# Kernel tuning notes

Measured on AMD Instinct MI355X. Metric: run time of the kernel, lower is better.

The kernel has to match this reference:

```python
import jax, jax.numpy as jnp
import numpy as np

B, S, H = 2, 1024, 4096
NH, NKV, HD = 32, 8, 128
GROUPS = NH // NKV  # 4


def _dequant_linear(x, w_q, scale, bias=None):
    # torch Linear layout: W [out, in]; per-output-channel symmetric dequant
    w = w_q.astype(jnp.float32) * scale[:, None]
    y = jnp.einsum('bsi,oi->bso', x, w)
    if bias is not None:
        y = y + bias
    return y


def setup_inputs() -> dict:
    key = jax.random.key(0)
    ks = jax.random.split(key, 12)
    hidden_states = jax.random.normal(ks[0], (B, S, H), dtype=jnp.float32)
    # additive causal mask: 0 on/below diagonal, large negative above
    causal = jnp.where(jnp.tril(jnp.ones((S, S), dtype=bool)), 0.0, -1e9).astype(jnp.float32)
    attention_mask = jnp.broadcast_to(causal[None, None], (B, 1, S, S))
    # int8-valued quantized weights, per-out-channel scales (~unit-variance effective weight rows / sqrt(fan_in))
    def qw(k, out, inp):
        return jax.random.randint(k, (out, inp), -127, 128, dtype=jnp.int32)
    def sc(k, out):
        return jax.random.uniform(k, (out,), dtype=jnp.float32, minval=1e-4, maxval=3e-4)
    wq_q = qw(ks[1], H, H);            wq_s = sc(ks[2], H)
    wk_q = qw(ks[3], NKV * HD, H);     wk_s = sc(ks[4], NKV * HD)
    wv_q = qw(ks[5], NKV * HD, H);     wv_s = sc(ks[6], NKV * HD)
    wo_q = qw(ks[7], H, H);            wo_s = sc(ks[8], H)
    bq = jax.random.normal(ks[9], (H,), dtype=jnp.float32) * 0.02
    bk = jax.random.normal(ks[10], (NKV * HD,), dtype=jnp.float32) * 0.02
    return {
        'hidden_states': hidden_states, 'attention_mask': attention_mask,
        'wq_q': wq_q, 'wq_s': wq_s, 'bq': bq,
        'wk_q': wk_q, 'wk_s': wk_s, 'bk': bk,
        'wv_q': wv_q, 'wv_s': wv_s,
        'wo_q': wo_q, 'wo_s': wo_s,
    }


def reference(hidden_states, attention_mask, wq_q, wq_s, bq, wk_q, wk_s, bk, wv_q, wv_s, wo_q, wo_s):
    bsz, q_len, _ = hidden_states.shape
    q = _dequant_linear(hidden_states, wq_q, wq_s, bq)      # [B,S,H]
    k = _dequant_linear(hidden_states, wk_q, wk_s, bk)      # [B,S,NKV*HD]
    v = _dequant_linear(hidden_states, wv_q, wv_s)          # [B,S,NKV*HD]
    q = q.reshape(bsz, q_len, NH, HD).transpose(0, 2, 1, 3)     # [B,NH,S,HD]
    k = k.reshape(bsz, q_len, NKV, HD).transpose(0, 2, 1, 3)    # [B,NKV,S,HD]
    v = v.reshape(bsz, q_len, NKV, HD).transpose(0, 2, 1, 3)
    # GQA: repeat_interleave kv heads along head dim
    k = jnp.repeat(k, GROUPS, axis=1)   # [B,NH,S,HD]
    v = jnp.repeat(v, GROUPS, axis=1)
    scores = jnp.einsum('bhqd,bhkd->bhqk', q, k) / np.float32(np.sqrt(HD))
    scores = scores + attention_mask
    attn = jax.nn.softmax(scores.astype(jnp.float32), axis=-1).astype(q.dtype)
    out = jnp.einsum('bhqk,bhkd->bhqd', attn, v)            # [B,NH,S,HD]
    out = out.transpose(0, 2, 1, 3).reshape(bsz, q_len, H)
    out = _dequant_linear(out, wo_q, wo_s)
    return out
```

## Files before the change

kernel.cpp:

```cpp
#include <hip/hip_runtime.h>
#include <math.h>

#define BB   2
#define SS   1024
#define HH   4096
#define NHH  32
#define NKVV 8
#define HDD  128
#define MR   2048
#define KVD  1024
#define NQKVD 6144
#define KD   4096
#define KHALF 2048
#define SCALE_F 0.08838834764831845f

typedef __attribute__((ext_vector_type(8))) short bf16x8;
typedef __attribute__((ext_vector_type(4))) float f32x4;
typedef __attribute__((ext_vector_type(4))) int i32x4;

#define MFMA(a, b, c) __builtin_amdgcn_mfma_f32_16x16x32_bf16((a), (b), (c), 0, 0, 0)
#define MFMA_I8(a, b, c) __builtin_amdgcn_mfma_i32_16x16x64_i8((a), (b), (c), 0, 0, 0)

__device__ __forceinline__ unsigned short f2bf(float f) {
  union { float f; unsigned u; } v; v.f = f;
  return (unsigned short)((v.u + 0x7fffu + ((v.u >> 16) & 1u)) >> 16);
}
__device__ __forceinline__ unsigned short f2h(float f) {
  union { _Float16 h; unsigned short s; } v; v.h = (_Float16)f; return v.s;
}
__device__ __forceinline__ float h2f(unsigned short s) {
  union { unsigned short s; _Float16 h; } v; v.s = s; return (float)v.h;
}
__device__ __forceinline__ float bf2f(unsigned short s) {
  union { unsigned u; float f; } v; v.u = ((unsigned)s) << 16; return v.f;
}
__device__ __forceinline__ float4 ld4h(const unsigned short* p) {
  uint2 d = *(const uint2*)p;
  float4 r;
  r.x = h2f((unsigned short)(d.x & 0xffff)); r.y = h2f((unsigned short)(d.x >> 16));
  r.z = h2f((unsigned short)(d.y & 0xffff)); r.w = h2f((unsigned short)(d.y >> 16));
  return r;
}

__device__ __forceinline__ void gload_lds16(const void* g, void* l) {
  __builtin_amdgcn_global_load_lds(
      (const __attribute__((address_space(1))) void*)g,
      (__attribute__((address_space(3))) void*)l, 16, 0, 0);
}

__device__ __forceinline__ signed char q8(float x, float inv) {
  float r = rintf(x * inv);
  r = fmaxf(-127.f, fminf(127.f, r));
  return (signed char)(int)r;
}

#define NQ16 ((size_t)HH * HH / 16)
#define NK16 ((size_t)KVD * HH / 16)
__global__ void cvt_w_all(const int* __restrict__ wq, const int* __restrict__ wk,
                          const int* __restrict__ wv, const int* __restrict__ wo,
                          signed char* __restrict__ wqkv, signed char* __restrict__ wo8) {
  size_t i = (size_t)blockIdx.x * 256 + threadIdx.x;
  const int* src;
  signed char* dst;
  if (i < NQ16) { src = wq; dst = wqkv; }
  else if (i < NQ16 + NK16) { src = wk - NQ16 * 16; dst = wqkv; }
  else if (i < NQ16 + 2 * NK16) { src = wv - (NQ16 + NK16) * 16; dst = wqkv; }
  else { src = wo - (NQ16 + 2 * NK16) * 16; dst = wo8 - (NQ16 + 2 * NK16) * 16; }
  const int4* p = (const int4*)(src + i * 16);
  union { signed char c[16]; int4 q; } o;
#pragma unroll
  for (int j = 0; j < 4; ++j) {
    int4 v = p[j];
    o.c[j * 4 + 0] = (signed char)v.x; o.c[j * 4 + 1] = (signed char)v.y;
    o.c[j * 4 + 2] = (signed char)v.z; o.c[j * 4 + 3] = (signed char)v.w;
  }
  *(int4*)(dst + i * 16) = o.q;
}

__global__ void quant_f32(const float* __restrict__ in, signed char* __restrict__ out,
                          float* __restrict__ scale) {
  __shared__ float wm[4];
  const int row = blockIdx.x;
  const int t = threadIdx.x;
  const float4* p = (const float4*)(in + (size_t)row * HH) + t * 4;
  float4 v[4];
  float m = 0.f;
#pragma unroll
  for (int j = 0; j < 4; ++j) {
    v[j] = p[j];
    m = fmaxf(m, fmaxf(fmaxf(fabsf(v[j].x), fabsf(v[j].y)), fmaxf(fabsf(v[j].z), fabsf(v[j].w))));
  }
#pragma unroll
  for (int o = 32; o; o >>= 1) m = fmaxf(m, __shfl_xor(m, o));
  if ((t & 63) == 0) wm[t >> 6] = m;
  __syncthreads();
  m = fmaxf(fmaxf(wm[0], wm[1]), fmaxf(wm[2], wm[3]));
  m = fmaxf(m, 1e-12f);
  const float inv = 127.f / m;
  union { signed char c[16]; int4 q; } o;
#pragma unroll
  for (int j = 0; j < 4; ++j) {
    o.c[j * 4 + 0] = q8(v[j].x, inv); o.c[j * 4 + 1] = q8(v[j].y, inv);
    o.c[j * 4 + 2] = q8(v[j].z, inv); o.c[j * 4 + 3] = q8(v[j].w, inv);
  }
  ((int4*)(out + (size_t)row * HH))[t] = o.q;
  if (t == 0) scale[row] = m / 127.f;
}

__global__ void quant_bf16(const unsigned short* __restrict__ in, signed char* __restrict__ out,
                           float* __restrict__ scale) {
  __shared__ float wm[4];
  const int row = blockIdx.x;
  const int t = threadIdx.x;
  const uint4* p = (const uint4*)(in + (size_t)row * HH) + t * 2;
  float f[16];
  float m = 0.f;
#pragma unroll
  for (int j = 0; j < 2; ++j) {
    uint4 d = p[j];
    unsigned u[4] = {d.x, d.y, d.z, d.w};
#pragma unroll
    for (int k = 0; k < 4; ++k) {
      f[j * 8 + k * 2] = bf2f((unsigned short)(u[k] & 0xffff));
      f[j * 8 + k * 2 + 1] = bf2f((unsigned short)(u[k] >> 16));
    }
  }
#pragma unroll
  for (int e = 0; e < 16; ++e) m = fmaxf(m, fabsf(f[e]));
#pragma unroll
  for (int o = 32; o; o >>= 1) m = fmaxf(m, __shfl_xor(m, o));
  if ((t & 63) == 0) wm[t >> 6] = m;
  __syncthreads();
  m = fmaxf(fmaxf(wm[0], wm[1]), fmaxf(wm[2], wm[3]));
  m = fmaxf(m, 1e-12f);
  const float inv = 127.f / m;
  union { signed char c[16]; int4 q; } o;
#pragma unroll
  for (int e = 0; e < 16; ++e) o.c[e] = q8(f[e], inv);
  ((int4*)(out + (size_t)row * HH))[t] = o.q;
  if (t == 0) scale[row] = m / 127.f;
}

template <int MODE>
__global__ __launch_bounds__(256) void gemm_i8(
    const signed char* __restrict__ A, const signed char* __restrict__ W,
    const float* __restrict__ sRow,
    const float* __restrict__ s0, const float* __restrict__ s1, const float* __restrict__ s2,
    unsigned short* __restrict__ P, int N) {
  __shared__ signed char ldsA[128 * 128];
  __shared__ signed char ldsB[128 * 128];
  const int t = threadIdx.x;
  const int lane = t & 63;
  const int w = t >> 6;
  const int wr = w & 1, wc = w >> 1;
  const int l15 = lane & 15, quad = lane >> 4;
  const int bm = blockIdx.y, bn = blockIdx.x, kz = blockIdx.z;

  const int srow_ = t >> 3;
  const int scol_ = ((t & 7) ^ (srow_ & 7)) * 16;
  const signed char* gA = A + (size_t)(bm * 128 + srow_) * KD + scol_ + kz * KHALF;
  const signed char* gW = W + (size_t)(bn * 128 + srow_) * KD + scol_ + kz * KHALF;
  signed char* lA = ldsA + t * 16;
  signed char* lB = ldsB + t * 16;

  i32x4 acc[4][4] = {};

  for (int k0 = 0; k0 < KHALF; k0 += 128) {
    __syncthreads();
#pragma unroll
    for (int j = 0; j < 4; ++j) {
      gload_lds16(gA + (size_t)j * 32 * KD + k0, lA + j * 4096);
      gload_lds16(gW + (size_t)j * 32 * KD + k0, lB + j * 4096);
    }
    __syncthreads();
#pragma unroll
    for (int kc = 0; kc < 2; ++kc) {
      i32x4 af[4], bfr[4];
#pragma unroll
      for (int mi = 0; mi < 4; ++mi) {
        const int row = wr * 64 + mi * 16 + l15;
        const int ch = (kc * 4 + quad) ^ (row & 7);
        af[mi] = *(const i32x4*)(ldsA + row * 128 + ch * 16);
      }
#pragma unroll
      for (int ni = 0; ni < 4; ++ni) {
        const int row = wc * 64 + ni * 16 + l15;
        const int ch = (kc * 4 + quad) ^ (row & 7);
        bfr[ni] = *(const i32x4*)(ldsB + row * 128 + ch * 16);
      }
#pragma unroll
      for (int mi = 0; mi < 4; ++mi)
#pragma unroll
        for (int ni = 0; ni < 4; ++ni)
          acc[mi][ni] = MFMA_I8(af[mi], bfr[ni], acc[mi][ni]);
    }
  }

  unsigned short* Pz = P + (size_t)kz * MR * N;
  const int row0 = bm * 128 + wr * 64 + quad * 4;
  const int col0 = bn * 128 + wc * 64 + l15;
#pragma unroll
  for (int ni = 0; ni < 4; ++ni) {
    const int col = col0 + ni * 16;
    float sc;
    if (MODE == 0)
      sc = (col < HH) ? s0[col] : (col < HH + KVD) ? s1[col - HH] : s2[col - HH - KVD];
    else
      sc = s0[col];
#pragma unroll
    for (int mi = 0; mi < 4; ++mi)
#pragma unroll
      for (int r = 0; r < 4; ++r) {
        const int row = row0 + mi * 16 + r;
        const float v = (float)acc[mi][ni][r] * sRow[row] * sc;
        Pz[(size_t)row * N + col] = f2h(v);
      }
  }
}

__global__ void epi_qkv(const unsigned short* __restrict__ P0, const unsigned short* __restrict__ P1,
                        const float* __restrict__ bQ, const float* __restrict__ bK,
                        unsigned short* __restrict__ oQ, unsigned short* __restrict__ oK,
                        unsigned short* __restrict__ oVt) {
  __shared__ unsigned short lds_t[64][65];
  const int t = threadIdx.x;
  int bid = blockIdx.x;
  if (bid < 10240) {
    const int row = bid / 5;
    const int col = (bid - row * 5) * 1024 + t * 4;
    const size_t off = (size_t)row * NQKVD + col;
    float4 a = ld4h(P0 + off), b2 = ld4h(P1 + off);
    union { unsigned short s[4]; uint2 d; } o;
    if (col < HH) {
      const float4 b = *(const float4*)(bQ + col);
      o.s[0] = f2bf((a.x + b2.x + b.x) * SCALE_F);
      o.s[1] = f2bf((a.y + b2.y + b.y) * SCALE_F);
      o.s[2] = f2bf((a.z + b2.z + b.z) * SCALE_F);
      o.s[3] = f2bf((a.w + b2.w + b.w) * SCALE_F);
      *(uint2*)(oQ + (size_t)row * HH + col) = o.d;
    } else {
      const int c = col - HH;
      const float4 b = *(const float4*)(bK + c);
      o.s[0] = f2bf(a.x + b2.x + b.x); o.s[1] = f2bf(a.y + b2.y + b.y);
      o.s[2] = f2bf(a.z + b2.z + b.z); o.s[3] = f2bf(a.w + b2.w + b.w);
      *(uint2*)(oK + (size_t)row * KVD + c) = o.d;
    }
  } else {
    bid -= 10240;
    const int c0 = (bid & 15) * 64;
    const int r0 = (bid >> 4) * 64;
    const int c4 = (t & 15) * 4;
#pragma unroll
    for (int rr = 0; rr < 4; ++rr) {
      const int rl = (t >> 4) * 4 + rr;
      const size_t off = (size_t)(r0 + rl) * NQKVD + (HH + KVD) + c0 + c4;
      float4 a = ld4h(P0 + off), b = ld4h(P1 + off);
      lds_t[c4 + 0][rl] = f2bf(a.x + b.x);
      lds_t[c4 + 1][rl] = f2bf(a.y + b.y);
      lds_t[c4 + 2][rl] = f2bf(a.z + b.z);
      lds_t[c4 + 3][rl] = f2bf(a.w + b.w);
    }
    __syncthreads();
    const int cl = t >> 2;
    const int rs = (t & 3) * 16;
    union { unsigned short s[16]; uint4 q[2]; } o;
#pragma unroll
    for (int i = 0; i < 16; ++i) o.s[i] = lds_t[cl][rs + i];
    uint4* dst = (uint4*)(oVt + (size_t)(c0 + cl) * MR + r0 + rs);
    dst[0] = o.q[0]; dst[1] = o.q[1];
  }
}

__global__ void epi_o(const unsigned short* __restrict__ P0, const unsigned short* __restrict__ P1,
                      float* __restrict__ out) {
  const int col = (blockIdx.x * 256 + threadIdx.x) * 4;
  const int row = blockIdx.y;
  const size_t off = (size_t)row * HH + col;
  float4 a = ld4h(P0 + off), b = ld4h(P1 + off);
  *(float4*)(out + off) = make_float4(a.x + b.x, a.y + b.y, a.z + b.z, a.w + b.w);
}

__global__ __launch_bounds__(256, 2) void attn_kernel(
    const unsigned short* __restrict__ Q,
    const unsigned short* __restrict__ K,
    const unsigned short* __restrict__ Vt,
    unsigned short* __restrict__ O) {
  __shared__ unsigned short ldsK[2][64][128];
  __shared__ unsigned short ldsV[2][2 * 128 * 32];
  __shared__ unsigned short ldsP[4][16 * 88];
  const int t = threadIdx.x;
  const int lane = t & 63;
  const int wv = t >> 6;
  const int l15 = lane & 15, quad = lane >> 4;
  const int qt = 15 - blockIdx.x;
  const int h = blockIdx.y;
  const int b = blockIdx.z;
  const int kv = h >> 2;
  const int q0w = qt * 64 + wv * 16;
  const int q = q0w + l15;

  bf16x8 bq[4];
  const unsigned short* qbase = Q + (size_t)(b * SS + q0w + l15) * HH + h * HDD + quad * 8;
#pragma unroll
  for (int kk = 0; kk < 4; ++kk) bq[kk] = *(const bf16x8*)(qbase + kk * 32);

  const int srow = t >> 4;
  const int schunk = (t & 15) ^ (srow & 7);
  const unsigned short* gK = K + (size_t)(b * SS + srow) * KVD + kv * HDD + schunk * 8;
  const unsigned short* gV = Vt + (size_t)(kv * HDD + wv * 32 + (lane >> 2)) * MR + b * SS + (lane & 3) * 8;
  unsigned short* lV = &ldsV[0][0] + wv * 1024 + lane * 8;
  unsigned short* lp = ldsP[wv];

  f32x4 accO[8] = {};
  float m_run = -1e30f, l_run = 0.f;

#pragma unroll
  for (int j = 0; j < 4; ++j)
    gload_lds16(gK + (size_t)j * 16 * KVD, &ldsK[0][j * 16][0] + t * 8);
#pragma unroll
  for (int kc = 0; kc < 2; ++kc)
#pragma unroll
    for (int j = 0; j < 2; ++j)
      gload_lds16(gV + (size_t)j * 16 * MR + kc * 32, lV + kc * 4096 + j * 512);
  __syncthreads();

  int cur = 0;
  for (int kt = 0; kt <= qt; ++kt) {
    const int k0 = kt * 64;
    if (kt < qt) {
#pragma unroll
      for (int j = 0; j < 4; ++j)
        gload_lds16(gK + (size_t)(k0 + 64 + j * 16) * KVD,
                    &ldsK[cur ^ 1][j * 16][0] + t * 8);
#pragma unroll
      for (int kc = 0; kc < 2; ++kc)
#pragma unroll
        for (int j = 0; j < 2; ++j)
          gload_lds16(gV + (size_t)j * 16 * MR + k0 + 64 + kc * 32,
                      lV + (cur ^ 1) * 8192 + kc * 4096 + j * 512);
    }

    f32x4 st[4] = {};
#pragma unroll
    for (int kk = 0; kk < 4; ++kk)
#pragma unroll
      for (int mf = 0; mf < 4; ++mf) {
        const int r = mf * 16 + l15;
        bf16x8 af = *(const bf16x8*)(&ldsK[cur][r][((kk * 4 + quad) ^ (r & 7)) * 8]);
        st[mf] = MFMA(af, bq[kk], st[mf]);
      }

    float p[4][4];
    float cm = -1e30f;
#pragma unroll
    for (int mf = 0; mf < 4; ++mf)
#pragma unroll
      for (int r = 0; r < 4; ++r) {
        const int k = k0 + mf * 16 + quad * 4 + r;
        float v = st[mf][r];
        if (k > q) v = -1e30f;
        p[mf][r] = v;
        cm = fmaxf(cm, v);
      }
    cm = fmaxf(cm, __shfl_xor(cm, 16));
    cm = fmaxf(cm, __shfl_xor(cm, 32));
    const float mn = fmaxf(m_run, cm);
    const float al = __expf(m_run - mn);
    float sum = 0.f;
#pragma unroll
    for (int mf = 0; mf < 4; ++mf)
#pragma unroll
      for (int r = 0; r < 4; ++r) {
        const float e = __expf(p[mf][r] - mn);
        p[mf][r] = e;
        sum += e;
      }
    sum += __shfl_xor(sum, 16);
    sum += __shfl_xor(sum, 32);
    l_run = l_run * al + sum;
    m_run = mn;
    float af4[4];
#pragma unroll
    for (int r = 0; r < 4; ++r) af4[r] = __shfl(al, quad * 4 + r);
#pragma unroll
    for (int cb = 0; cb < 8; ++cb)
#pragma unroll
      for (int r = 0; r < 4; ++r) accO[cb][r] *= af4[r];

#pragma unroll
    for (int mf = 0; mf < 4; ++mf) {
      union { unsigned short s[4]; unsigned long long d; } pk;
#pragma unroll
      for (int r = 0; r < 4; ++r) pk.s[r] = f2bf(p[mf][r]);
      *(unsigned long long*)(lp + l15 * 88 + mf * 16 + quad * 4) = pk.d;
    }
    bf16x8 ap0 = *(const bf16x8*)(lp + l15 * 88 + quad * 8);
    bf16x8 ap1 = *(const bf16x8*)(lp + l15 * 88 + 32 + quad * 8);

#pragma unroll
    for (int cb = 0; cb < 8; ++cb) {
      bf16x8 bv0 = *(const bf16x8*)(&ldsV[cur][0] + (cb * 16 + l15) * 32 + quad * 8);
      bf16x8 bv1 = *(const bf16x8*)(&ldsV[cur][0] + 4096 + (cb * 16 + l15) * 32 + quad * 8);
      accO[cb] = MFMA(ap0, bv0, accO[cb]);
      accO[cb] = MFMA(ap1, bv1, accO[cb]);
    }

    __syncthreads();
    cur ^= 1;
  }

  float lr[4];
#pragma unroll
  for (int r = 0; r < 4; ++r) lr[r] = __shfl(l_run, quad * 4 + r);
  unsigned short* ob = O + (size_t)(b * SS + q0w + quad * 4) * HH + h * HDD + l15;
#pragma unroll
  for (int cb = 0; cb < 8; ++cb)
#pragma unroll
    for (int r = 0; r < 4; ++r)
      ob[(size_t)r * HH + cb * 16] = f2bf(accO[cb][r] / lr[r]);
}

extern "C" void kernel_launch(void* const* d_in, const int* in_sizes, int n_in,
                              void* d_out, int out_size, void* d_ws, size_t ws_size,
                              hipStream_t stream) {
  const float* x = (const float*)d_in[0];
  const int* wq = (const int*)d_in[2];
  const float* wqs = (const float*)d_in[3];
  const float* bq = (const float*)d_in[4];
  const int* wk = (const int*)d_in[5];
  const float* wks = (const float*)d_in[6];
  const float* bk = (const float*)d_in[7];
  const int* wv = (const int*)d_in[8];
  const float* wvs = (const float*)d_in[9];
  const int* wo = (const int*)d_in[10];
  const float* wos = (const float*)d_in[11];
  float* out = (float*)d_out;
  char* ws = (char*)d_ws;

  signed char*    x_i8    = (signed char*)   (ws + (0ull   << 20));
  signed char*    wqkv_i8 = (signed char*)   (ws + (8ull   << 20));
  signed char*    wo_i8   = (signed char*)   (ws + (32ull  << 20));
  unsigned short* Pq      = (unsigned short*)(ws + (48ull  << 20));
  unsigned short* q_bf    = (unsigned short*)(ws + (0ull   << 20));
  unsigned short* k_bf    = (unsigned short*)(ws + (16ull  << 20));
  unsigned short* v_t     = (unsigned short*)(ws + (20ull  << 20));
  unsigned short* a_bf    = (unsigned short*)(ws + (48ull  << 20));
  signed char*    a_i8    = (signed char*)   (ws + (64ull  << 20));
  unsigned short* Po      = (unsigned short*)(ws + (96ull  << 20));
  float*          sx      = (float*)         (ws + (128ull << 20));
  float*          sa      = (float*)         (ws + (129ull << 20));
  if (ws_size < (130ull << 20)) return;

  quant_f32<<<MR, 256, 0, stream>>>(x, x_i8, sx);
  cvt_w_all<<<10240, 256, 0, stream>>>(wq, wk, wv, wo, wqkv_i8, wo_i8);

  gemm_i8<0><<<dim3(NQKVD / 128, MR / 128, 2), 256, 0, stream>>>(
      x_i8, wqkv_i8, sx, wqs, wks, wvs, Pq, NQKVD);

  epi_qkv<<<10752, 256, 0, stream>>>(Pq, Pq + (size_t)MR * NQKVD, bq, bk, q_bf, k_bf, v_t);

  attn_kernel<<<dim3(16, NHH, BB), 256, 0, stream>>>(q_bf, k_bf, v_t, a_bf);

  quant_bf16<<<MR, 256, 0, stream>>>(a_bf, a_i8, sa);
  gemm_i8<1><<<dim3(HH / 128, MR / 128, 2), 256, 0, stream>>>(
      a_i8, wo_i8, sa, wos, nullptr, nullptr, Po, HH);
  epi_o<<<dim3(4, MR), 256, 0, stream>>>(Po, Po + (size_t)MR * HH, out);
}
```

Baseline: 428.1 us.

## Streamline flash-attention softmax with exp2, lazy rescale, deferred sum, and priorities

Folds log2(e) into the Q scale so the softmax can use the raw v_exp_f32 exp2 instruction, and applies the causal mask only on the diagonal tile. The running max and accumulator are rescaled only when some row's max grows by more than a threshold (8 in log2 units). The row-sum reduction across lanes is moved out of the loop to run once at the end. It also packs bf16 with v_cvt_pk_bf16_f32 and raises wave priority around the MFMA blocks. Together these cut VALU, shuffle and exp work in the attention inner loop, in exchange for small changes to numerics (unnormalized exponents can reach 2^8 before a rescale) and reliance on inline asm.

```diff
diff --git a/kernel.cpp b/kernel.cpp
--- a/kernel.cpp
+++ b/kernel.cpp
@@ -12,7 +12,7 @@
 #define NQKVD 6144
 #define KD   4096
 #define KHALF 2048
-#define SCALE_F 0.08838834764831845f
+#define SCALE2_F 0.12751744f
 
 typedef __attribute__((ext_vector_type(8))) short bf16x8;
 typedef __attribute__((ext_vector_type(4))) float f32x4;
@@ -40,6 +40,12 @@
   r.x = h2f((unsigned short)(d.x & 0xffff)); r.y = h2f((unsigned short)(d.x >> 16));
   r.z = h2f((unsigned short)(d.y & 0xffff)); r.w = h2f((unsigned short)(d.y >> 16));
   return r;
+}
+__device__ __forceinline__ float exp2_fast(float x) {
+  float r; asm("v_exp_f32 %0, %1" : "=v"(r) : "v"(x)); return r;
+}
+__device__ __forceinline__ unsigned cvt_pk_bf16(float a, float b) {
+  unsigned r; asm("v_cvt_pk_bf16_f32 %0, %1, %2" : "=v"(r) : "v"(a), "v"(b)); return r;
 }
 
 __device__ __forceinline__ void gload_lds16(const void* g, void* l) {
@@ -233,10 +239,10 @@
     union { unsigned short s[4]; uint2 d; } o;
     if (col < HH) {
       const float4 b = *(const float4*)(bQ + col);
-      o.s[0] = f2bf((a.x + b2.x + b.x) * SCALE_F);
-      o.s[1] = f2bf((a.y + b2.y + b.y) * SCALE_F);
-      o.s[2] = f2bf((a.z + b2.z + b.z) * SCALE_F);
-      o.s[3] = f2bf((a.w + b2.w + b.w) * SCALE_F);
+      o.s[0] = f2bf((a.x + b2.x + b.x) * SCALE2_F);
+      o.s[1] = f2bf((a.y + b2.y + b.y) * SCALE2_F);
+      o.s[2] = f2bf((a.z + b2.z + b.z) * SCALE2_F);
+      o.s[3] = f2bf((a.w + b2.w + b.w) * SCALE2_F);
       *(uint2*)(oQ + (size_t)row * HH + col) = o.d;
     } else {
       const int c = col - HH;
@@ -312,7 +318,7 @@
   unsigned short* lp = ldsP[wv];
 
   f32x4 accO[8] = {};
-  float m_run = -1e30f, l_run = 0.f;
+  float m_run = -1e30f, l_part = 0.f;
 
 #pragma unroll
   for (int j = 0; j < 4; ++j)
@@ -341,6 +347,7 @@
     }
 
     f32x4 st[4] = {};
+    __builtin_amdgcn_s_setprio(1);
 #pragma unroll
     for (int kk = 0; kk < 4; ++kk)
 #pragma unroll
@@ -349,54 +356,60 @@
         bf16x8 af = *(const bf16x8*)(&ldsK[cur][r][((kk * 4 + quad) ^ (r & 7)) * 8]);
         st[mf] = MFMA(af, bq[kk], st[mf]);
       }
+    __builtin_amdgcn_s_setprio(0);
 
     float p[4][4];
+#pragma unroll
+    for (int mf = 0; mf < 4; ++mf)
+#pragma unroll
+      for (int r = 0; r < 4; ++r) p[mf][r] = st[mf][r];
+    if (kt == qt) {
+#pragma unroll
+      for (int mf = 0; mf < 4; ++mf)
+#pragma unroll
+        for (int r = 0; r < 4; ++r) {
+          const int k = k0 + mf * 16 + quad * 4 + r;
+          if (k > q) p[mf][r] = -1e30f;
+        }
+    }
     float cm = -1e30f;
 #pragma unroll
     for (int mf = 0; mf < 4; ++mf)
 #pragma unroll
-      for (int r = 0; r < 4; ++r) {
-        const int k = k0 + mf * 16 + quad * 4 + r;
-        float v = st[mf][r];
-        if (k > q) v = -1e30f;
-        p[mf][r] = v;
-        cm = fmaxf(cm, v);
-      }
+      for (int r = 0; r < 4; ++r) cm = fmaxf(cm, p[mf][r]);
     cm = fmaxf(cm, __shfl_xor(cm, 16));
     cm = fmaxf(cm, __shfl_xor(cm, 32));
-    const float mn = fmaxf(m_run, cm);
-    const float al = __expf(m_run - mn);
-    float sum = 0.f;
-#pragma unroll
-    for (int mf = 0; mf < 4; ++mf)
-#pragma unroll
-      for (int r = 0; r < 4; ++r) {
-        const float e = __expf(p[mf][r] - mn);
-        p[mf][r] = e;
-        sum += e;
-      }
-    sum += __shfl_xor(sum, 16);
-    sum += __shfl_xor(sum, 32);
-    l_run = l_run * al + sum;
-    m_run = mn;
-    float af4[4];
-#pragma unroll
-    for (int r = 0; r < 4; ++r) af4[r] = __shfl(al, quad * 4 + r);
-#pragma unroll
-    for (int cb = 0; cb < 8; ++cb)
-#pragma unroll
-      for (int r = 0; r < 4; ++r) accO[cb][r] *= af4[r];
+
+    if (!__all(cm <= m_run + 8.f)) {
+      const float mn = fmaxf(m_run, cm);
+      const float al = exp2_fast(m_run - mn);
+      l_part *= al;
+      m_run = mn;
+      float af4[4];
+#pragma unroll
+      for (int r = 0; r < 4; ++r) af4[r] = __shfl(al, quad * 4 + r);
+#pragma unroll
+      for (int cb = 0; cb < 8; ++cb)
+#pragma unroll
+        for (int r = 0; r < 4; ++r) accO[cb][r] *= af4[r];
+    }
 
 #pragma unroll
     for (int mf = 0; mf < 4; ++mf) {
-      union { unsigned short s[4]; unsigned long long d; } pk;
-#pragma unroll
-      for (int r = 0; r < 4; ++r) pk.s[r] = f2bf(p[mf][r]);
+      const float e0 = exp2_fast(p[mf][0] - m_run);
+      const float e1 = exp2_fast(p[mf][1] - m_run);
+      const float e2 = exp2_fast(p[mf][2] - m_run);
+      const float e3 = exp2_fast(p[mf][3] - m_run);
+      l_part += (e0 + e1) + (e2 + e3);
+      union { unsigned u[2]; unsigned long long d; } pk;
+      pk.u[0] = cvt_pk_bf16(e0, e1);
+      pk.u[1] = cvt_pk_bf16(e2, e3);
       *(unsigned long long*)(lp + l15 * 88 + mf * 16 + quad * 4) = pk.d;
     }
     bf16x8 ap0 = *(const bf16x8*)(lp + l15 * 88 + quad * 8);
     bf16x8 ap1 = *(const bf16x8*)(lp + l15 * 88 + 32 + quad * 8);
 
+    __builtin_amdgcn_s_setprio(1);
 #pragma unroll
     for (int cb = 0; cb < 8; ++cb) {
       bf16x8 bv0 = *(const bf16x8*)(&ldsV[cur][0] + (cb * 16 + l15) * 32 + quad * 8);
@@ -404,14 +417,17 @@
       accO[cb] = MFMA(ap0, bv0, accO[cb]);
       accO[cb] = MFMA(ap1, bv1, accO[cb]);
     }
+    __builtin_amdgcn_s_setprio(0);
 
     __syncthreads();
     cur ^= 1;
   }
 
+  l_part += __shfl_xor(l_part, 16);
+  l_part += __shfl_xor(l_part, 32);
   float lr[4];
 #pragma unroll
-  for (int r = 0; r < 4; ++r) lr[r] = __shfl(l_run, quad * 4 + r);
+  for (int r = 0; r < 4; ++r) lr[r] = __shfl(l_part, quad * 4 + r);
   unsigned short* ob = O + (size_t)(b * SS + q0w + quad * 4) * HH + h * HDD + l15;
 #pragma unroll
   for (int cb = 0; cb < 8; ++cb)
```

New measurement: 424.8 us. No clear change (-0.8%).
